# Optimization experiments

Hardware: AMD Instinct MI355X
Metric: run time of the kernel (lower is better)

The kernel has to match this reference:

```python
import jax, jax.numpy as jnp
import numpy as np

NEG_BIG = -9.0e15  # mask value from original code (-9000000000000000.0)


def setup_inputs() -> dict:
    key = jax.random.key(0)
    k1, k2, k3, k4, k5 = jax.random.split(key, 5)
    B, N, M, D = 32, 1024, 1024, 128
    input1 = jax.random.normal(k1, (B, N, D), dtype=jnp.float32)
    input2 = jax.random.normal(k2, (B, M, D), dtype=jnp.float32)
    adj = jax.random.randint(k3, (B, N, M), 0, 2, dtype=jnp.int32)
    # xavier_normal on (D,1): std = gain*sqrt(2/(fan_in+fan_out)) = 1.414*sqrt(2/(D+1))
    std = 1.414 * np.sqrt(2.0 / (D + 1))
    a1 = jax.random.normal(k4, (D, 1), dtype=jnp.float32) * std
    a2 = jax.random.normal(k5, (D, 1), dtype=jnp.float32) * std
    return {"input1": input1, "input2": input2, "adj": adj, "a1": a1, "a2": a2}


def reference(input1, input2, adj, a1, a2):
    h, g = input1, input2
    # e1: (B,N,1), e2: (B,1,M); broadcast add replaces the repeat() calls
    e1 = jnp.matmul(h, a1)                      # (B,N,1)
    e2 = jnp.matmul(g, a2).transpose(0, 2, 1)   # (B,1,M)
    e = jax.nn.leaky_relu(e1 + e2, negative_slope=0.2)  # (B,N,M)
    attention = jnp.where(adj > 0, e, NEG_BIG)
    attention = jax.nn.softmax(attention, axis=2)
    attention = jnp.where(jnp.isnan(attention), 0.0, attention)
    # per-batch loop in original builds adj_[b,i,j] = adj[b,i,:].sum(); vectorized:
    deg = jnp.sum(adj, axis=2, keepdims=True).astype(attention.dtype)  # (B,N,1)
    attention = attention * deg
    h_prime = jnp.matmul(attention, g)          # (B,N,D)
    return h_prime
```

## Files before the change

kernel.cpp:

```cpp
#include <hip/hip_runtime.h>

#define BB 32
#define NN 1024
#define MM 1024
#define DD 128

typedef __attribute__((ext_vector_type(4))) float f32x4;
typedef __attribute__((ext_vector_type(8))) __bf16 bf16x8;
typedef unsigned short ushort_t;
typedef unsigned int uint_t;

#define L2E 1.44269504f

__device__ __forceinline__ unsigned f2bf(float x) {
    unsigned u = __builtin_bit_cast(unsigned, x);
    return (u + 0x7fffu + ((u >> 16) & 1u)) >> 16;
}

#define GLOAD16(gp, lp)                                                     \
    __builtin_amdgcn_global_load_lds(                                       \
        (const __attribute__((address_space(1))) unsigned int*)(gp),        \
        (__attribute__((address_space(3))) unsigned int*)(lp), 16, 0, 0)

__global__ __launch_bounds__(256) void prep(
    const float* __restrict__ g, const float* __restrict__ h,
    const float* __restrict__ a1, const float* __restrict__ a2,
    ushort_t* __restrict__ gq, float* __restrict__ e1,
    float* __restrict__ e2B, float* __restrict__ e2D)
{
    __shared__ ushort_t tl[DD][66];
    int b = blockIdx.y, m0 = blockIdx.x * 64, t = threadIdx.x;

    #pragma unroll
    for (int i = 0; i < 8; i++) {
        int idx = i * 256 + t;
        int m = idx >> 5;
        int c4 = (idx & 31) * 4;
        float4 v = *(const float4*)(h + ((size_t)(b * NN + m0 + m)) * DD + c4);
        float4 av = *(const float4*)(a1 + c4);
        float p = v.x * av.x + v.y * av.y + v.z * av.z + v.w * av.w;
        #pragma unroll
        for (int s = 16; s; s >>= 1) p += __shfl_xor(p, s);
        if ((t & 31) == 0) e1[b * NN + m0 + m] = p;
    }
    #pragma unroll
    for (int i = 0; i < 8; i++) {
        int idx = i * 256 + t;
        int m = idx >> 5;
        int c4 = (idx & 31) * 4;
        float4 v = *(const float4*)(g + ((size_t)(b * MM + m0 + m)) * DD + c4);
        tl[c4 + 0][m] = (ushort_t)f2bf(v.x);
        tl[c4 + 1][m] = (ushort_t)f2bf(v.y);
        tl[c4 + 2][m] = (ushort_t)f2bf(v.z);
        tl[c4 + 3][m] = (ushort_t)f2bf(v.w);
        float4 av = *(const float4*)(a2 + c4);
        float p = v.x * av.x + v.y * av.y + v.z * av.z + v.w * av.w;
        #pragma unroll
        for (int s = 16; s; s >>= 1) p += __shfl_xor(p, s);
        if ((t & 31) == 0) {
            e2B[b * MM + m0 + m] = __builtin_amdgcn_exp2f(L2E * p);
            e2D[b * MM + m0 + m] = __builtin_amdgcn_exp2f(0.2f * L2E * p);
        }
    }
    __syncthreads();
    #pragma unroll
    for (int i = 0; i < 4; i++) {
        int idx = i * 256 + t;
        int d = idx >> 3;
        int c = (idx & 7) * 8;
        int4 o;
        o.x = (int)((unsigned)tl[d][c + 0] | ((unsigned)tl[d][c + 1] << 16));
        o.y = (int)((unsigned)tl[d][c + 2] | ((unsigned)tl[d][c + 3] << 16));
        o.z = (int)((unsigned)tl[d][c + 4] | ((unsigned)tl[d][c + 5] << 16));
        o.w = (int)((unsigned)tl[d][c + 6] | ((unsigned)tl[d][c + 7] << 16));
        int mg = m0 + c;
        *(int4*)(gq + (((size_t)((b * 32 + (mg >> 5)) * DD + d)) << 5) + (mg & 31)) = o;
    }
}

__global__ __launch_bounds__(256, 2) void attn_tiled(
    const int* __restrict__ adj, const ushort_t* __restrict__ gq,
    const float* __restrict__ e1, const float* __restrict__ e2B,
    const float* __restrict__ e2D, float* __restrict__ out)
{
    __shared__ __align__(16) float BfS[MM];
    __shared__ __align__(16) float DfS[MM];
    __shared__ __align__(16) int adjS[2][64 * 64];
    __shared__ __align__(16) ushort_t gqS[2][2 * 128 * 32];

    int b = blockIdx.y, n0 = blockIdx.x * 64, t = threadIdx.x;
    int wid = t >> 6, lane = t & 63;
    int rlo = lane & 15, hh = lane >> 4;
    int r = wid * 16 + rlo;

    *(float4*)(&BfS[t * 4]) = *(const float4*)(e2B + b * MM + t * 4);
    *(float4*)(&DfS[t * 4]) = *(const float4*)(e2D + b * MM + t * 4);
    float e1r = e1[b * NN + n0 + r];
    float An   = __builtin_amdgcn_exp2f(L2E * e1r);
    float Cn   = __builtin_amdgcn_exp2f(0.2f * L2E * e1r);
    float invA = __builtin_amdgcn_exp2f(-L2E * e1r);
    __syncthreads();

    const int* adjb = adj + (size_t)(b * NN + n0) * MM;
    const ushort_t* gqb = gq + (size_t)b * (32 * DD * 32);

    int adi[4], aoff[4];
    #pragma unroll
    for (int i = 0; i < 4; i++) {
        adi[i] = t + i * 256;
        int arow = adi[i] >> 4, aseg = (adi[i] & 15) ^ (arow & 15);
        aoff[i] = arow * MM + aseg * 4;
    }
    int gtile[4], goff[4];
    #pragma unroll
    for (int i = 0; i < 4; i++) {
        int di = t + i * 256;
        gtile[i] = di >> 9;
        int idx = di & 511;
        int gd = idx >> 2, gseg = (idx & 3) ^ ((gd >> 1) & 3);
        goff[i] = gd * 32 + gseg * 8;
    }

#define STAGE(P, K) do {                                                    \
        _Pragma("unroll")                                                   \
        for (int i = 0; i < 4; i++)                                         \
            GLOAD16(adjb + (size_t)aoff[i] + (K) * 64,                      \
                    &adjS[P][adi[i] * 4]);                                  \
        _Pragma("unroll")                                                   \
        for (int i = 0; i < 4; i++)                                         \
            GLOAD16(gqb + (size_t)(2 * (K) + gtile[i]) * 4096 + goff[i],    \
                    &gqS[P][(t + i * 256) * 8]);                            \
    } while (0)

    f32x4 acc[8];
    #pragma unroll
    for (int j = 0; j < 8; j++) acc[j] = (f32x4){0.f, 0.f, 0.f, 0.f};
    float zl = 0.f;
    int dcnt = 0;

#define KSTEP(P, K, KS) do {                                                \
        int4 a0 = *(const int4*)(                                           \
            &adjS[P][r * 64 + (((KS) * 8 + 2 * hh) ^ rlo) * 4]);            \
        int4 a1 = *(const int4*)(                                           \
            &adjS[P][r * 64 + (((KS) * 8 + 2 * hh + 1) ^ rlo) * 4]);        \
        int mo = (K) * 64 + (KS) * 32 + 8 * hh;                             \
        float4 b0 = *(const float4*)(&BfS[mo]);                             \
        float4 b1 = *(const float4*)(&BfS[mo + 4]);                         \
        float4 d0 = *(const float4*)(&DfS[mo]);                             \
        float4 d1 = *(const float4*)(&DfS[mo + 4]);                         \
        float Bv[8] = {b0.x, b0.y, b0.z, b0.w, b1.x, b1.y, b1.z, b1.w};     \
        float Dv[8] = {d0.x, d0.y, d0.z, d0.w, d1.x, d1.y, d1.z, d1.w};     \
        int   ax[8] = {a0.x, a0.y, a0.z, a0.w, a1.x, a1.y, a1.z, a1.w};     \
        bf16x8 af;                                                          \
        _Pragma("unroll")                                                   \
        for (int jj = 0; jj < 8; jj++) {                                    \
            float val = (Bv[jj] > invA) ? Bv[jj] * An : Dv[jj] * Cn;        \
            float wv = (ax[jj] > 0) ? val : 0.f;                            \
            zl += wv;                                                       \
            dcnt += ax[jj];                                                 \
            af[jj] = (__bf16)wv;                                            \
        }                                                                   \
        _Pragma("unroll")                                                   \
        for (int j = 0; j < 8; j++) {                                       \
            int d = j * 16 + rlo;                                           \
            int4 bv = *(const int4*)(&gqS[P][(KS) * 4096 + d * 32 +         \
                                             (hh ^ ((rlo >> 1) & 3)) * 8]); \
            acc[j] = __builtin_amdgcn_mfma_f32_16x16x32_bf16(               \
                         af, __builtin_bit_cast(bf16x8, bv), acc[j], 0,0,0);\
        }                                                                   \
    } while (0)

    STAGE(0, 0);

    for (int k = 0; k < 16; ++k) {
        asm volatile("s_waitcnt vmcnt(0)" ::: "memory");
        __builtin_amdgcn_s_barrier();
        __builtin_amdgcn_sched_barrier(0);
        if (k < 15) STAGE((k + 1) & 1, k + 1);
        KSTEP(k & 1, k, 0);
        KSTEP(k & 1, k, 1);
    }

#undef KSTEP
#undef STAGE

    zl += __shfl_xor(zl, 16); zl += __shfl_xor(zl, 32);
    dcnt += __shfl_xor(dcnt, 16); dcnt += __shfl_xor(dcnt, 32);
    float sc = (dcnt > 0) ? ((float)dcnt / zl) : 0.f;

    float scr[4];
    #pragma unroll
    for (int rg = 0; rg < 4; rg++) scr[rg] = __shfl(sc, 4 * hh + rg);

    float* ob = out + ((size_t)(b * NN + n0 + wid * 16)) * DD + rlo;
    #pragma unroll
    for (int j = 0; j < 8; j++)
        #pragma unroll
        for (int rg = 0; rg < 4; rg++)
            ob[(size_t)(4 * hh + rg) * DD + j * 16] = acc[j][rg] * scr[rg];
}

extern "C" void kernel_launch(void* const* d_in, const int* in_sizes, int n_in,
                              void* d_out, int out_size, void* d_ws, size_t ws_size,
                              hipStream_t stream) {
    const float* h   = (const float*)d_in[0];
    const float* g   = (const float*)d_in[1];
    const int*   adj = (const int*)d_in[2];
    const float* a1  = (const float*)d_in[3];
    const float* a2  = (const float*)d_in[4];
    float* out = (float*)d_out;

    char* ws = (char*)d_ws;
    float*    e1  = (float*)(ws);
    float*    e2B = (float*)(ws + (128u << 10));
    float*    e2D = (float*)(ws + (256u << 10));
    ushort_t* gq  = (ushort_t*)(ws + (512u << 10));

    prep<<<dim3(MM / 64, BB), 256, 0, stream>>>(g, h, a1, a2, gq, e1, e2B, e2D);
    attn_tiled<<<dim3(NN / 64, BB), 256, 0, stream>>>(adj, gq, e1, e2B, e2D, out);
}
```

Measured before the change: 50.28 us.

## Prepack adjacency rows into bitmasks in LDS before the main loop

Instead of streaming int32 adjacency tiles into double-buffered LDS each k-step, each wave loads its 16 full adjacency rows up front, packs them into 1-bit masks using shuffles, and computes row degrees once. The main loop then reads a single mask word per k-step and only stages the bf16 g tiles asynchronously. This cuts LDS footprint and per-step LDS traffic, which may allow better occupancy. The cost is that the adjacency load is no longer overlapped with MFMA work, so a serialized prologue now holds the 4 MB-per-batch int reads.

```diff
diff --git a/kernel.cpp b/kernel.cpp
--- a/kernel.cpp
+++ b/kernel.cpp
@@ -85,7 +85,8 @@
 {
     __shared__ __align__(16) float BfS[MM];
     __shared__ __align__(16) float DfS[MM];
-    __shared__ __align__(16) int adjS[2][64 * 64];
+    __shared__ __align__(16) uint_t maskS[64 * 32];
+    __shared__ float degS[64];
     __shared__ __align__(16) ushort_t gqS[2][2 * 128 * 32];
 
     int b = blockIdx.y, n0 = blockIdx.x * 64, t = threadIdx.x;
@@ -99,18 +100,49 @@
     float An   = __builtin_amdgcn_exp2f(L2E * e1r);
     float Cn   = __builtin_amdgcn_exp2f(0.2f * L2E * e1r);
     float invA = __builtin_amdgcn_exp2f(-L2E * e1r);
-    __syncthreads();
 
     const int* adjb = adj + (size_t)(b * NN + n0) * MM;
     const ushort_t* gqb = gq + (size_t)b * (32 * DD * 32);
 
-    int adi[4], aoff[4];
-    #pragma unroll
-    for (int i = 0; i < 4; i++) {
-        adi[i] = t + i * 256;
-        int arow = adi[i] >> 4, aseg = (adi[i] & 15) ^ (arow & 15);
-        aoff[i] = arow * MM + aseg * 4;
-    }
+#define PACKROW(ROW, V0, V1, V2, V3) do {                                   \
+        int cnt = 0; int sw = 2 * ((ROW) & 15);                             \
+        int4 vv[4] = {V0, V1, V2, V3};                                      \
+        _Pragma("unroll")                                                   \
+        for (int rr = 0; rr < 4; rr++) {                                    \
+            uint_t nib = (vv[rr].x > 0 ? 1u:0u) | (vv[rr].y > 0 ? 2u:0u)    \
+                       | (vv[rr].z > 0 ? 4u:0u) | (vv[rr].w > 0 ? 8u:0u);   \
+            cnt += __popc(nib);                                             \
+            uint_t val = nib << (4 * (lane & 7));                           \
+            val |= __shfl_xor(val, 1);                                      \
+            val |= __shfl_xor(val, 2);                                      \
+            val |= __shfl_xor(val, 4);                                      \
+            if ((lane & 7) == 0)                                            \
+                maskS[(ROW) * 32 + ((rr * 8 + (lane >> 3)) ^ sw)] = val;    \
+        }                                                                   \
+        _Pragma("unroll")                                                   \
+        for (int s = 32; s; s >>= 1) cnt += __shfl_xor(cnt, s);             \
+        if (lane == 0) degS[ROW] = (float)cnt;                              \
+    } while (0)
+
+    #pragma unroll 1
+    for (int i = 0; i < 16; i += 2) {
+        int row0 = wid * 16 + i, row1 = row0 + 1;
+        const int* ap0 = adjb + (size_t)row0 * MM + lane * 4;
+        const int* ap1 = adjb + (size_t)row1 * MM + lane * 4;
+        int4 u0 = *(const int4*)(ap0);
+        int4 u1 = *(const int4*)(ap0 + 256);
+        int4 u2 = *(const int4*)(ap0 + 512);
+        int4 u3 = *(const int4*)(ap0 + 768);
+        int4 w0 = *(const int4*)(ap1);
+        int4 w1 = *(const int4*)(ap1 + 256);
+        int4 w2 = *(const int4*)(ap1 + 512);
+        int4 w3 = *(const int4*)(ap1 + 768);
+        PACKROW(row0, u0, u1, u2, u3);
+        PACKROW(row1, w0, w1, w2, w3);
+    }
+#undef PACKROW
+    __syncthreads();
+
     int gtile[4], goff[4];
     #pragma unroll
     for (int i = 0; i < 4; i++) {
@@ -124,10 +156,6 @@
 #define STAGE(P, K) do {                                                    \
         _Pragma("unroll")                                                   \
         for (int i = 0; i < 4; i++)                                         \
-            GLOAD16(adjb + (size_t)aoff[i] + (K) * 64,                      \
-                    &adjS[P][adi[i] * 4]);                                  \
-        _Pragma("unroll")                                                   \
-        for (int i = 0; i < 4; i++)                                         \
             GLOAD16(gqb + (size_t)(2 * (K) + gtile[i]) * 4096 + goff[i],    \
                     &gqS[P][(t + i * 256) * 8]);                            \
     } while (0)
@@ -136,13 +164,10 @@
     #pragma unroll
     for (int j = 0; j < 8; j++) acc[j] = (f32x4){0.f, 0.f, 0.f, 0.f};
     float zl = 0.f;
-    int dcnt = 0;
 
 #define KSTEP(P, K, KS) do {                                                \
-        int4 a0 = *(const int4*)(                                           \
-            &adjS[P][r * 64 + (((KS) * 8 + 2 * hh) ^ rlo) * 4]);            \
-        int4 a1 = *(const int4*)(                                           \
-            &adjS[P][r * 64 + (((KS) * 8 + 2 * hh + 1) ^ rlo) * 4]);        \
+        uint_t mw = maskS[r * 32 + ((2 * (K) + (KS)) ^ (2 * rlo))];         \
+        uint_t mby = (mw >> (8 * hh)) & 0xffu;                              \
         int mo = (K) * 64 + (KS) * 32 + 8 * hh;                             \
         float4 b0 = *(const float4*)(&BfS[mo]);                             \
         float4 b1 = *(const float4*)(&BfS[mo + 4]);                         \
@@ -150,14 +175,12 @@
         float4 d1 = *(const float4*)(&DfS[mo + 4]);                         \
         float Bv[8] = {b0.x, b0.y, b0.z, b0.w, b1.x, b1.y, b1.z, b1.w};     \
         float Dv[8] = {d0.x, d0.y, d0.z, d0.w, d1.x, d1.y, d1.z, d1.w};     \
-        int   ax[8] = {a0.x, a0.y, a0.z, a0.w, a1.x, a1.y, a1.z, a1.w};     \
         bf16x8 af;                                                          \
         _Pragma("unroll")                                                   \
         for (int jj = 0; jj < 8; jj++) {                                    \
             float val = (Bv[jj] > invA) ? Bv[jj] * An : Dv[jj] * Cn;        \
-            float wv = (ax[jj] > 0) ? val : 0.f;                            \
+            float wv = ((mby >> jj) & 1u) ? val : 0.f;                      \
             zl += wv;                                                       \
-            dcnt += ax[jj];                                                 \
             af[jj] = (__bf16)wv;                                            \
         }                                                                   \
         _Pragma("unroll")                                                   \
@@ -185,8 +208,8 @@
 #undef STAGE
 
     zl += __shfl_xor(zl, 16); zl += __shfl_xor(zl, 32);
-    dcnt += __shfl_xor(dcnt, 16); dcnt += __shfl_xor(dcnt, 32);
-    float sc = (dcnt > 0) ? ((float)dcnt / zl) : 0.f;
+    float dgv = degS[r];
+    float sc = (dgv > 0.f) ? (dgv / zl) : 0.f;
 
     float scr[4];
     #pragma unroll
```

Measured after the change: 55.68 us. +10.8%, slower.

## Load adjacency in 64x256 chunks and triple-buffer gq with two-deep prefetch

Applied to the files above, without the earlier changes.

Adjacency tiles now go into one large 64x256 LDS buffer, refilled once every four k-steps, instead of being double-buffered in 64x64 pieces each step. The gq tiles move to a three-slot ring that is prefetched two steps ahead. The aim is fewer barriers and larger, better-coalesced adjacency transfers, plus deeper latency hiding for the B operand. In exchange, LDS use rises enough that launch bounds drop to one block per CU. Each adjacency refill also stalls compute, because that buffer is single-buffered.

```diff
diff --git a/kernel.cpp b/kernel.cpp
--- a/kernel.cpp
+++ b/kernel.cpp
@@ -78,15 +78,15 @@
     }
 }
 
-__global__ __launch_bounds__(256, 2) void attn_tiled(
+__global__ __launch_bounds__(256, 1) void attn_tiled(
     const int* __restrict__ adj, const ushort_t* __restrict__ gq,
     const float* __restrict__ e1, const float* __restrict__ e2B,
     const float* __restrict__ e2D, float* __restrict__ out)
 {
     __shared__ __align__(16) float BfS[MM];
     __shared__ __align__(16) float DfS[MM];
-    __shared__ __align__(16) int adjS[2][64 * 64];
-    __shared__ __align__(16) ushort_t gqS[2][2 * 128 * 32];
+    __shared__ __align__(16) int adjS[64 * 256];
+    __shared__ __align__(16) ushort_t gqS[3][2 * 128 * 32];
 
     int b = blockIdx.y, n0 = blockIdx.x * 64, t = threadIdx.x;
     int wid = t >> 6, lane = t & 63;
@@ -99,18 +99,22 @@
     float An   = __builtin_amdgcn_exp2f(L2E * e1r);
     float Cn   = __builtin_amdgcn_exp2f(0.2f * L2E * e1r);
     float invA = __builtin_amdgcn_exp2f(-L2E * e1r);
-    __syncthreads();
 
     const int* adjb = adj + (size_t)(b * NN + n0) * MM;
     const ushort_t* gqb = gq + (size_t)b * (32 * DD * 32);
 
-    int adi[4], aoff[4];
-    #pragma unroll
-    for (int i = 0; i < 4; i++) {
-        adi[i] = t + i * 256;
-        int arow = adi[i] >> 4, aseg = (adi[i] & 15) ^ (arow & 15);
-        aoff[i] = arow * MM + aseg * 4;
-    }
+#define FILL(SC) do {                                                       \
+        _Pragma("unroll")                                                   \
+        for (int i = 0; i < 16; i++) {                                      \
+            int slot = t + i * 256;                                         \
+            int row = slot >> 6;                                            \
+            int seg = slot & 63;                                            \
+            int swz = seg ^ (row & 15);                                     \
+            GLOAD16(adjb + (size_t)row * MM + (SC) * 256 + swz * 4,         \
+                    &adjS[slot * 4]);                                       \
+        }                                                                   \
+    } while (0)
+
     int gtile[4], goff[4];
     #pragma unroll
     for (int i = 0; i < 4; i++) {
@@ -121,14 +125,10 @@
         goff[i] = gd * 32 + gseg * 8;
     }
 
-#define STAGE(P, K) do {                                                    \
+#define GST(P, C) do {                                                      \
         _Pragma("unroll")                                                   \
         for (int i = 0; i < 4; i++)                                         \
-            GLOAD16(adjb + (size_t)aoff[i] + (K) * 64,                      \
-                    &adjS[P][adi[i] * 4]);                                  \
-        _Pragma("unroll")                                                   \
-        for (int i = 0; i < 4; i++)                                         \
-            GLOAD16(gqb + (size_t)(2 * (K) + gtile[i]) * 4096 + goff[i],    \
+            GLOAD16(gqb + (size_t)(2 * (C) + gtile[i]) * 4096 + goff[i],    \
                     &gqS[P][(t + i * 256) * 8]);                            \
     } while (0)
 
@@ -138,19 +138,21 @@
     float zl = 0.f;
     int dcnt = 0;
 
-#define KSTEP(P, K, KS) do {                                                \
+#define KSTEP(GB, C, KS) do {                                               \
+        int js = ((C) & 3) * 2 + (KS);                                      \
         int4 a0 = *(const int4*)(                                           \
-            &adjS[P][r * 64 + (((KS) * 8 + 2 * hh) ^ rlo) * 4]);            \
-        int4 a1 = *(const int4*)(                                           \
-            &adjS[P][r * 64 + (((KS) * 8 + 2 * hh + 1) ^ rlo) * 4]);        \
-        int mo = (K) * 64 + (KS) * 32 + 8 * hh;                             \
+            &adjS[r * 256 + ((js * 8 + 2 * hh) ^ rlo) * 4]);                \
+        int4 a1v = *(const int4*)(                                          \
+            &adjS[r * 256 + ((js * 8 + 2 * hh + 1) ^ rlo) * 4]);            \
+        int mo = (C) * 64 + (KS) * 32 + 8 * hh;                             \
         float4 b0 = *(const float4*)(&BfS[mo]);                             \
         float4 b1 = *(const float4*)(&BfS[mo + 4]);                         \
         float4 d0 = *(const float4*)(&DfS[mo]);                             \
         float4 d1 = *(const float4*)(&DfS[mo + 4]);                         \
         float Bv[8] = {b0.x, b0.y, b0.z, b0.w, b1.x, b1.y, b1.z, b1.w};     \
         float Dv[8] = {d0.x, d0.y, d0.z, d0.w, d1.x, d1.y, d1.z, d1.w};     \
-        int   ax[8] = {a0.x, a0.y, a0.z, a0.w, a1.x, a1.y, a1.z, a1.w};     \
+        int   ax[8] = {a0.x, a0.y, a0.z, a0.w,                              \
+                       a1v.x, a1v.y, a1v.z, a1v.w};                         \
         bf16x8 af;                                                          \
         _Pragma("unroll")                                                   \
         for (int jj = 0; jj < 8; jj++) {                                    \
@@ -163,26 +165,45 @@
         _Pragma("unroll")                                                   \
         for (int j = 0; j < 8; j++) {                                       \
             int d = j * 16 + rlo;                                           \
-            int4 bv = *(const int4*)(&gqS[P][(KS) * 4096 + d * 32 +         \
-                                             (hh ^ ((rlo >> 1) & 3)) * 8]); \
+            int4 bv = *(const int4*)(&(GB)[(KS) * 4096 + d * 32 +           \
+                                           (hh ^ ((rlo >> 1) & 3)) * 8]);   \
             acc[j] = __builtin_amdgcn_mfma_f32_16x16x32_bf16(               \
                          af, __builtin_bit_cast(bf16x8, bv), acc[j], 0,0,0);\
         }                                                                   \
     } while (0)
 
-    STAGE(0, 0);
-
-    for (int k = 0; k < 16; ++k) {
-        asm volatile("s_waitcnt vmcnt(0)" ::: "memory");
-        __builtin_amdgcn_s_barrier();
-        __builtin_amdgcn_sched_barrier(0);
-        if (k < 15) STAGE((k + 1) & 1, k + 1);
-        KSTEP(k & 1, k, 0);
-        KSTEP(k & 1, k, 1);
+    FILL(0);
+    GST(0, 0);
+    GST(1, 1);
+    asm volatile("s_waitcnt vmcnt(4) lgkmcnt(0)" ::: "memory");
+    __builtin_amdgcn_s_barrier();
+    __builtin_amdgcn_sched_barrier(0);
+
+    #pragma unroll 1
+    for (int c = 0; c < 16; ++c) {
+        if (c > 0) {
+            if (c == 15) asm volatile("s_waitcnt vmcnt(0)" ::: "memory");
+            else         asm volatile("s_waitcnt vmcnt(4)" ::: "memory");
+            __builtin_amdgcn_s_barrier();
+            __builtin_amdgcn_sched_barrier(0);
+        }
+        if (c == 4 || c == 8 || c == 12) {
+            FILL(c >> 2);
+            if (c + 2 < 16) GST((c + 2) % 3, c + 2);
+            asm volatile("s_waitcnt vmcnt(4)" ::: "memory");
+            __builtin_amdgcn_s_barrier();
+            __builtin_amdgcn_sched_barrier(0);
+        } else {
+            if (c + 2 < 16) GST((c + 2) % 3, c + 2);
+        }
+        ushort_t* gb = &gqS[c % 3][0];
+        KSTEP(gb, c, 0);
+        KSTEP(gb, c, 1);
     }
 
 #undef KSTEP
-#undef STAGE
+#undef GST
+#undef FILL
 
     zl += __shfl_xor(zl, 16); zl += __shfl_xor(zl, 32);
     dcnt += __shfl_xor(dcnt, 16); dcnt += __shfl_xor(dcnt, 32);
```

Measured after the change: 69.04 us. 1.37x slower.
